# Performance work log

Hardware: AMD Instinct MI355X
Metric: run time of the kernel (lower is better)

## Reference

```python
import jax, jax.numpy as jnp
import numpy as np

N = 50000   # num entities
R2 = 480    # num_rels * 2
D = 200     # h_dim
T = 4       # sequence_len (graph snapshots)
E = 100000  # edges per snapshot
L = 2       # rgcn layers
SLOPE = (1.0 / 8.0 + 1.0 / 3.0) / 2.0  # deterministic rrelu (eval-mode expected slope)


def setup_inputs() -> dict:
    key = jax.random.key(0)
    ks = jax.random.split(key, 13)
    s = 1.0 / np.sqrt(D)
    w = lambda k, shp, sc: jax.random.normal(k, shp, dtype=jnp.float32) * sc
    return {
        "src": jax.random.randint(ks[0], (T, E), 0, N, dtype=jnp.int32),
        "dst": jax.random.randint(ks[1], (T, E), 0, N, dtype=jnp.int32),
        "etype": jax.random.randint(ks[2], (T, E), 0, R2, dtype=jnp.int32),
        "dynamic_emb": w(ks[3], (N, D), 1.0),
        "emb_rel": w(ks[4], (R2, D), s),
        "W_ih": w(ks[5], (3 * D, 2 * D), s),
        "W_hh": w(ks[6], (3 * D, D), s),
        "b_ih": jnp.zeros((3 * D,), jnp.float32),
        "b_hh": jnp.zeros((3 * D,), jnp.float32),
        "W_neighbor": w(ks[7], (L, D, D), s),
        "W_loop": w(ks[8], (L, D, D), s),
        "time_gate_weight": w(ks[9], (D, D), s),
        "time_gate_bias": jnp.zeros((D,), jnp.float32),
    }


def _l2norm(x):
    n = jnp.linalg.norm(x, axis=-1, keepdims=True)
    return x / jnp.maximum(n, 1e-12)


def _gru(x, hprev, W_ih, W_hh, b_ih, b_hh):
    gi = x @ W_ih.T + b_ih
    gh = hprev @ W_hh.T + b_hh
    ir, iz, inn = jnp.split(gi, 3, axis=-1)
    hr, hz, hn = jnp.split(gh, 3, axis=-1)
    r = jax.nn.sigmoid(ir + hr)
    z = jax.nn.sigmoid(iz + hz)
    n = jnp.tanh(inn + r * hn)
    return (1.0 - z) * n + z * hprev


def reference(src, dst, etype, dynamic_emb, emb_rel, W_ih, W_hh, b_ih, b_hh,
              W_neighbor, W_loop, time_gate_weight, time_gate_bias):
    h_init = _l2norm(dynamic_emb)  # layer_norm=True path (F.normalize)

    def step(carry, g):
        h, h0 = carry
        s, d_, et = g
        # per-relation mean of entity embeddings touching that relation (r_to_e spans)
        ent_idx = jnp.concatenate([s, d_])          # [2E]
        seg = jnp.concatenate([et, et])             # [2E]
        ssum = jax.ops.segment_sum(h[ent_idx], seg, num_segments=R2)
        cnt = jax.ops.segment_sum(jnp.ones_like(seg, jnp.float32), seg, num_segments=R2)
        x_mean = ssum / jnp.maximum(cnt, 1.0)[:, None]          # absent rels stay 0
        x_input = jnp.concatenate([emb_rel, x_mean], axis=1)    # [R2, 2D]
        h0 = _l2norm(_gru(x_input, h0, W_ih, W_hh, b_ih, b_hh))
        # UnionRGCNLayer x L: gather -> sum-aggregate -> norm + self-loop -> rrelu
        deg = jax.ops.segment_sum(jnp.ones_like(d_, jnp.float32), d_, num_segments=N)
        norm = 1.0 / jnp.maximum(deg, 1.0)
        hh = h
        for l in range(L):
            pre = hh[s] + h0[et]                                  # [E, D]
            agg = jax.ops.segment_sum(pre, d_, num_segments=N) @ W_neighbor[l]
            out = agg * norm[:, None] + hh @ W_loop[l]
            hh = jnp.where(out >= 0, out, out * SLOPE)            # rrelu (eval)
        cur = _l2norm(hh)
        tw = jax.nn.sigmoid(h @ time_gate_weight + time_gate_bias)
        h = tw * cur + (1.0 - tw) * h
        return (h, h0), h

    (_, _), hist = jax.lax.scan(step, (h_init, emb_rel), (src, dst, etype))
    return hist  # [T, N, D] history of evolved entity embeddings
```

## Files before the change

### kernel.cpp

```cpp
#include <hip/hip_runtime.h>
#include <math.h>

#define NE 50000
#define R2C 480
#define DD 200
#define TT 4
#define EE 100000
#define SLOPE 0.22916666666666666f

#define SCCH 8
#define EPB (256 * SCCH)
#define APAD 224
#define WPAD 224
#define WSZ (208 * WPAD)
#define DCH 4096
#define DNC ((NE + DCH - 1) / DCH)
#define RSPL 8

typedef short short8 __attribute__((ext_vector_type(8)));
typedef float float4v __attribute__((ext_vector_type(4)));

__device__ __forceinline__ float sigm(float x) { return 1.f / (1.f + expf(-x)); }

__device__ __forceinline__ short f2bf(float f) {
  union { float f; unsigned u; } v;
  v.f = f;
  unsigned r = v.u + 0x7fffu + ((v.u >> 16) & 1u);
  return (short)(r >> 16);
}


__global__ void init_h_kernel(const float* __restrict__ emb, float* __restrict__ h) {
  int n = blockIdx.x;
  int lane = threadIdx.x;
  size_t base = (size_t)n * DD;
  float v0 = emb[base + lane];
  float v1 = emb[base + 64 + lane];
  float v2 = emb[base + 128 + lane];
  float v3 = (lane < 8) ? emb[base + 192 + lane] : 0.f;
  float ss = v0 * v0 + v1 * v1 + v2 * v2 + v3 * v3;
#pragma unroll
  for (int off = 32; off; off >>= 1) ss += __shfl_down(ss, off);
  ss = __shfl(ss, 0);
  float inv = 1.f / fmaxf(sqrtf(ss), 1e-12f);
  h[base + lane] = v0 * inv;
  h[base + 64 + lane] = v1 * inv;
  h[base + 128 + lane] = v2 * inv;
  if (lane < 8) h[base + 192 + lane] = v3 * inv;
}

__global__ void copy_kernel(const float* __restrict__ a, float* __restrict__ b, int n) {
  int i = blockIdx.x * blockDim.x + threadIdx.x;
  if (i < n) b[i] = a[i];
}

__global__ void fill_x_kernel(const float* __restrict__ emb_rel, float* __restrict__ X) {
  int i = blockIdx.x * blockDim.x + threadIdx.x;
  if (i >= R2C * DD) return;
  int r = i / DD, d = i - r * DD;
  X[(size_t)r * 400 + d] = emb_rel[i];
}

__global__ void prep_w_kernel(const float* __restrict__ Wnb, const float* __restrict__ Wlp,
                              const float* __restrict__ Wtg, short* __restrict__ Wb) {
  int idx = blockIdx.x * 256 + threadIdx.x;
  if (idx >= 5 * WSZ) return;
  int m = idx / WSZ, rem = idx - m * WSZ;
  int n = rem / WPAD, k = rem - n * WPAD;
  const float* s;
  if (m == 0) s = Wnb;
  else if (m == 1) s = Wnb + DD * DD;
  else if (m == 2) s = Wlp;
  else if (m == 3) s = Wlp + DD * DD;
  else s = Wtg;
  float v = (n < DD && k < DD) ? s[(size_t)k * DD + n] : 0.f;
  Wb[idx] = f2bf(v);
}

__global__ __launch_bounds__(256) void hist_kernel(const int* __restrict__ et,
                                                   const int* __restrict__ dst,
                                                   int* __restrict__ et_hist,
                                                   int* __restrict__ deg_hist) {
  __shared__ int lh[R2C];
  int t = blockIdx.y;
  int tid = threadIdx.x;
  int e0 = blockIdx.x * EPB;
  for (int i = tid; i < R2C; i += 256) lh[i] = 0;
  __syncthreads();
#pragma unroll
  for (int c = 0; c < SCCH; c++) {
    int e = e0 + c * 256 + tid;
    if (e < EE) {
      atomicAdd(&lh[et[(size_t)t * EE + e]], 1);
      atomicAdd(&deg_hist[(size_t)t * NE + dst[(size_t)t * EE + e]], 1);
    }
  }
  __syncthreads();
  for (int i = tid; i < R2C; i += 256)
    if (lh[i]) atomicAdd(&et_hist[t * R2C + i], lh[i]);
}

__global__ void scan_rel_kernel(const int* __restrict__ et_hist, int* __restrict__ rowptr) {
  int t = blockIdx.x;
  int tid = threadIdx.x;
  __shared__ int s[512];
  int v = (tid < R2C) ? 2 * et_hist[t * R2C + tid] : 0;
  s[tid] = v;
  __syncthreads();
  for (int off = 1; off < 512; off <<= 1) {
    int x = (tid >= off) ? s[tid - off] : 0;
    __syncthreads();
    s[tid] += x;
    __syncthreads();
  }
  if (tid < R2C) rowptr[t * (R2C + 1) + tid] = s[tid] - v;
  if (tid == 0) rowptr[t * (R2C + 1) + R2C] = 2 * EE;
}

__global__ __launch_bounds__(256) void deg_partial_kernel(const int* __restrict__ deg_hist,
                                                          int* __restrict__ csum) {
  int t = blockIdx.y, c = blockIdx.x, tid = threadIdx.x;
  const int* dh = deg_hist + (size_t)t * NE;
  int base = c * DCH + tid * 16;
  int s = 0;
  if (base < NE) {
    int end = base + 16 > NE ? NE : base + 16;
    for (int i = base; i < end; i++) s += dh[i];
  }
  __shared__ int red[256];
  red[tid] = s;
  __syncthreads();
  for (int off = 128; off; off >>= 1) {
    if (tid < off) red[tid] += red[tid + off];
    __syncthreads();
  }
  if (tid == 0) csum[t * DNC + c] = red[0];
}

__global__ __launch_bounds__(256) void deg_emit_kernel(const int* __restrict__ deg_hist,
                                                       const int* __restrict__ csum,
                                                       int* __restrict__ rowptr,
                                                       float* __restrict__ normv) {
  int t = blockIdx.y, c = blockIdx.x, tid = threadIdx.x;
  const int* dh = deg_hist + (size_t)t * NE;
  __shared__ int scan[256];
  __shared__ int soff;
  int base = c * DCH + tid * 16;
  int s = 0;
  if (base < NE) {
    int end = base + 16 > NE ? NE : base + 16;
    for (int i = base; i < end; i++) s += dh[i];
  }
  scan[tid] = s;
  __syncthreads();
  for (int off = 1; off < 256; off <<= 1) {
    int x = (tid >= off) ? scan[tid - off] : 0;
    __syncthreads();
    scan[tid] += x;
    __syncthreads();
  }
  if (tid == 0) {
    int o = 0;
    for (int j = 0; j < c; j++) o += csum[t * DNC + j];
    soff = o;
  }
  __syncthreads();
  int run = soff + scan[tid] - s;
  if (base < NE) {
    int end = base + 16 > NE ? NE : base + 16;
    for (int i = base; i < end; i++) {
      int v = dh[i];
      rowptr[t * (NE + 1) + i] = run;
      normv[(size_t)t * NE + i] = 1.f / fmaxf((float)v, 1.f);
      run += v;
    }
  }
  if (c == 0 && tid == 0) rowptr[t * (NE + 1) + NE] = EE;
}

__global__ __launch_bounds__(256) void scatter_rel_kernel(const int* __restrict__ src,
                                                          const int* __restrict__ dst,
                                                          const int* __restrict__ et,
                                                          const int* __restrict__ rowptr,
                                                          int* __restrict__ cursor,
                                                          int* __restrict__ sorted_ent) {
  __shared__ int lcnt[R2C];
  __shared__ int lbase[R2C];
  int t = blockIdx.y;
  int tid = threadIdx.x;
  int e0 = blockIdx.x * EPB;
  for (int i = tid; i < R2C; i += 256) lcnt[i] = 0;
  __syncthreads();
  int rels[SCCH];
#pragma unroll
  for (int c = 0; c < SCCH; c++) {
    int e = e0 + c * 256 + tid;
    int r = (e < EE) ? et[(size_t)t * EE + e] : -1;
    rels[c] = r;
    if (r >= 0) atomicAdd(&lcnt[r], 2);
  }
  __syncthreads();
  const int* rp = rowptr + t * (R2C + 1);
  for (int i = tid; i < R2C; i += 256) {
    int c = lcnt[i];
    lbase[i] = rp[i] + (c ? atomicAdd(&cursor[t * R2C + i], c) : 0);
    lcnt[i] = 0;
  }
  __syncthreads();
  int* se = sorted_ent + (size_t)t * 2 * EE;
#pragma unroll
  for (int c = 0; c < SCCH; c++) {
    int r = rels[c];
    if (r >= 0) {
      int e = e0 + c * 256 + tid;
      int off = atomicAdd(&lcnt[r], 2);
      int p = lbase[r] + off;
      se[p] = src[(size_t)t * EE + e];
      se[p + 1] = dst[(size_t)t * EE + e];
    }
  }
}

__global__ void scatter_dst_kernel(const int* __restrict__ src, const int* __restrict__ dst,
                                   const int* __restrict__ et, const int* __restrict__ rowptr,
                                   int* __restrict__ cursor, int2* __restrict__ sorted_se) {
  int i = blockIdx.x * blockDim.x + threadIdx.x;
  if (i >= TT * EE) return;
  int t = i / EE;
  int d = dst[i];
  int base = rowptr[t * (NE + 1) + d];
  int p = base + atomicAdd(&cursor[(size_t)t * NE + d], 1);
  sorted_se[(size_t)t * EE + p] = make_int2(src[i], et[i]);
}


__global__ void relmean_part_kernel(const float* __restrict__ h, const int* __restrict__ rowptr,
                                    const int* __restrict__ sorted_ent_t,
                                    float* __restrict__ Xpart) {
  int r = blockIdx.x, j = blockIdx.y;
  int beg = rowptr[r], end = rowptr[r + 1];
  int lane = threadIdx.x & 63, w = threadIdx.x >> 6;
  float a0 = 0, a1 = 0, a2 = 0, a3 = 0;
  for (int i = beg + j * 4 + w; i < end; i += 4 * RSPL) {
    int idx = sorted_ent_t[i];
    const float* row = h + (size_t)idx * DD;
    a0 += row[lane];
    a1 += row[64 + lane];
    a2 += row[128 + lane];
    if (lane < 8) a3 += row[192 + lane];
  }
  __shared__ float part[4][DD];
  part[w][lane] = a0;
  part[w][64 + lane] = a1;
  part[w][128 + lane] = a2;
  if (lane < 8) part[w][192 + lane] = a3;
  __syncthreads();
  for (int d = threadIdx.x; d < DD; d += 256) {
    Xpart[((size_t)r * RSPL + j) * DD + d] = part[0][d] + part[1][d] + part[2][d] + part[3][d];
  }
}

__global__ void relmean_comb_kernel(const float* __restrict__ Xpart,
                                    const int* __restrict__ rowptr, float* __restrict__ X) {
  int r = blockIdx.x;
  int d = threadIdx.x;
  if (d >= DD) return;
  float s = 0.f;
#pragma unroll
  for (int j = 0; j < RSPL; j++) s += Xpart[((size_t)r * RSPL + j) * DD + d];
  float cnt = fmaxf((float)(rowptr[r + 1] - rowptr[r]), 1.f);
  X[(size_t)r * 400 + 200 + d] = s / cnt;
}

__global__ __launch_bounds__(256) void gemm_gru(const float* __restrict__ X,
                                                const float* __restrict__ h0,
                                                const float* __restrict__ W_ih,
                                                const float* __restrict__ W_hh,
                                                float* __restrict__ gi) {
  int z = blockIdx.z;
  const float* A = z ? h0 : X;
  const float* B = z ? W_hh : W_ih;
  float* C = gi + (size_t)z * R2C * 600;
  int K = z ? DD : 2 * DD;
  const int M = R2C, N = 600;
  __shared__ float As[32][33];
  __shared__ float Bs[32][33];
  int tid = threadIdx.x;
  int col0 = blockIdx.x * 32;
  int row0 = blockIdx.y * 32;
  int tr = tid >> 4, tc = tid & 15;
  float a00 = 0, a01 = 0, a10 = 0, a11 = 0;
  for (int k0 = 0; k0 < K; k0 += 32) {
    __syncthreads();
    for (int i = tid; i < 1024; i += 256) {
      int kk = i & 31, r = i >> 5;
      int row = row0 + r, k = k0 + kk;
      As[kk][r] = (row < M && k < K) ? A[(size_t)row * K + k] : 0.f;
    }
    for (int i = tid; i < 1024; i += 256) {
      int kk = i & 31, c = i >> 5;
      int col = col0 + c, k = k0 + kk;
      Bs[kk][c] = (col < N && k < K) ? B[(size_t)col * K + k] : 0.f;
    }
    __syncthreads();
#pragma unroll
    for (int kk = 0; kk < 32; kk++) {
      float x0 = As[kk][tr * 2], x1 = As[kk][tr * 2 + 1];
      float y0 = Bs[kk][tc * 2], y1 = Bs[kk][tc * 2 + 1];
      a00 += x0 * y0;
      a01 += x0 * y1;
      a10 += x1 * y0;
      a11 += x1 * y1;
    }
  }
  int row = row0 + tr * 2, col = col0 + tc * 2;
  if (row < M && col < N) C[(size_t)row * N + col] = a00;
  if (row < M && col + 1 < N) C[(size_t)row * N + col + 1] = a01;
  if (row + 1 < M && col < N) C[(size_t)(row + 1) * N + col] = a10;
  if (row + 1 < M && col + 1 < N) C[(size_t)(row + 1) * N + col + 1] = a11;
}

__global__ void gru_gate_kernel(const float* __restrict__ gi, const float* __restrict__ gh,
                                const float* __restrict__ b_ih, const float* __restrict__ b_hh,
                                float* __restrict__ h0) {
  int r = blockIdx.x;
  int tid = threadIdx.x;
  int lane = tid & 63, w = tid >> 6;
  __shared__ float red[4];
  float o = 0.f;
  if (tid < DD) {
    size_t b = (size_t)r * (3 * DD);
    float ir = gi[b + tid] + b_ih[tid];
    float iz = gi[b + DD + tid] + b_ih[DD + tid];
    float inn = gi[b + 2 * DD + tid] + b_ih[2 * DD + tid];
    float hr = gh[b + tid] + b_hh[tid];
    float hz = gh[b + DD + tid] + b_hh[DD + tid];
    float hn = gh[b + 2 * DD + tid] + b_hh[2 * DD + tid];
    float hv = h0[(size_t)r * DD + tid];
    float rr = sigm(ir + hr);
    float z = sigm(iz + hz);
    float n = tanhf(inn + rr * hn);
    o = (1.f - z) * n + z * hv;
  }
  float ss = o * o;
#pragma unroll
  for (int off = 32; off; off >>= 1) ss += __shfl_down(ss, off);
  if (lane == 0) red[w] = ss;
  __syncthreads();
  float tot = red[0] + red[1] + red[2] + red[3];
  float inv = 1.f / fmaxf(sqrtf(tot), 1e-12f);
  if (tid < DD) h0[(size_t)r * DD + tid] = o * inv;
}

__global__ void agg_kernel(const float* __restrict__ hh, const float* __restrict__ h0,
                           const int* __restrict__ rowptr, const int2* __restrict__ se_t,
                           const float* __restrict__ normv_t, short* __restrict__ aggb) {
  int w = threadIdx.x >> 6, lane = threadIdx.x & 63;
  int n = blockIdx.x * 4 + w;
  if (n >= NE) return;
  int beg = rowptr[n], end = rowptr[n + 1];
  float a0 = 0, a1 = 0, a2 = 0, a3 = 0;
  for (int i = beg; i < end; i++) {
    int2 p = se_t[i];
    const float* hr = hh + (size_t)p.x * DD;
    const float* qr = h0 + (size_t)p.y * DD;
    a0 += hr[lane] + qr[lane];
    a1 += hr[64 + lane] + qr[64 + lane];
    a2 += hr[128 + lane] + qr[128 + lane];
    if (lane < 8) a3 += hr[192 + lane] + qr[192 + lane];
  }
  float nm = normv_t[n];
  short* outp = aggb + (size_t)n * APAD;
  outp[lane] = f2bf(a0 * nm);
  outp[64 + lane] = f2bf(a1 * nm);
  outp[128 + lane] = f2bf(a2 * nm);
  if (lane < 8) outp[192 + lane] = f2bf(a3 * nm);
  else if (lane < 32) outp[192 + lane] = 0;
}


__global__ __launch_bounds__(256) void gemm_l0(const short* __restrict__ A1,
                                               const float* __restrict__ A2,
                                               const short* __restrict__ WbN,
                                               const short* __restrict__ WbL,
                                               const short* __restrict__ WbT,
                                               float* __restrict__ C, float* __restrict__ tg) {
  __shared__ short Bt[3][208][40];
  int tid = threadIdx.x;
  int lane = tid & 63, w = tid >> 6;
  int quad = lane >> 4, l16 = lane & 15;
  int row = blockIdx.x * 64 + w * 16 + l16;
  bool rok = row < NE;

  short8 af1[7], af2[7];
#pragma unroll
  for (int c = 0; c < 7; c++) {
    af1[c] = rok ? *(const short8*)(A1 + (size_t)row * APAD + c * 32 + quad * 8)
                 : (short8){0, 0, 0, 0, 0, 0, 0, 0};
  }
#pragma unroll
  for (int c = 0; c < 7; c++) {
    int kb = c * 32 + quad * 8;
    short8 a = (short8){0, 0, 0, 0, 0, 0, 0, 0};
    if (rok && kb < DD) {
      const float* ap = A2 + (size_t)row * DD + kb;
      float4v v0 = *(const float4v*)ap;
      float4v v1 = *(const float4v*)(ap + 4);
      short tmp[8] = {f2bf(v0[0]), f2bf(v0[1]), f2bf(v0[2]), f2bf(v0[3]),
                      f2bf(v1[0]), f2bf(v1[1]), f2bf(v1[2]), f2bf(v1[3])};
      a = *(short8*)&tmp[0];
    }
    af2[c] = a;
  }

  float4v accA[13], accT[13];
#pragma unroll
  for (int ct = 0; ct < 13; ct++) {
    accA[ct] = (float4v){0.f, 0.f, 0.f, 0.f};
    accT[ct] = (float4v){0.f, 0.f, 0.f, 0.f};
  }

#pragma unroll
  for (int c = 0; c < 7; c++) {
    __syncthreads();
#pragma unroll
    for (int it = 0; it < 10; it++) {
      int s = tid + it * 256;
      if (s < 2496) {
        int m = s / 832;
        int ss = s - m * 832;
        int n = ss % 208, k8 = (ss / 208) * 8;
        const short* Wb = (m == 0) ? WbN : (m == 1) ? WbL : WbT;
        *(short8*)&Bt[m][n][k8] = *(const short8*)&Wb[(size_t)n * WPAD + c * 32 + k8];
      }
    }
    __syncthreads();
#pragma unroll
    for (int ct = 0; ct < 13; ct++) {
      short8 b0 = *(short8*)&Bt[0][ct * 16 + l16][quad * 8];
      short8 b1 = *(short8*)&Bt[1][ct * 16 + l16][quad * 8];
      short8 b2 = *(short8*)&Bt[2][ct * 16 + l16][quad * 8];
      accA[ct] = __builtin_amdgcn_mfma_f32_16x16x32_bf16(af1[c], b0, accA[ct], 0, 0, 0);
      accA[ct] = __builtin_amdgcn_mfma_f32_16x16x32_bf16(af2[c], b1, accA[ct], 0, 0, 0);
      accT[ct] = __builtin_amdgcn_mfma_f32_16x16x32_bf16(af2[c], b2, accT[ct], 0, 0, 0);
    }
  }
  int r0 = blockIdx.x * 64 + w * 16 + quad * 4;
#pragma unroll
  for (int ct = 0; ct < 13; ct++) {
    int col = ct * 16 + l16;
    if (col >= DD) continue;
#pragma unroll
    for (int i = 0; i < 4; i++) {
      int r = r0 + i;
      if (r < NE) {
        float v = accA[ct][i];
        v = (v >= 0.f) ? v : v * SLOPE;
        C[(size_t)r * DD + col] = v;
        tg[(size_t)r * DD + col] = accT[ct][i];
      }
    }
  }
}

__global__ __launch_bounds__(256) void gemm_l1(const short* __restrict__ A1,
                                               const float* __restrict__ A2,
                                               const short* __restrict__ WbN,
                                               const short* __restrict__ WbL,
                                               const float* __restrict__ tg,
                                               const float* __restrict__ tgb,
                                               const float* __restrict__ hcur,
                                               float* __restrict__ outp) {
  __shared__ short Bt[2][208][40];
  int tid = threadIdx.x;
  int lane = tid & 63, w = tid >> 6;
  int quad = lane >> 4, l16 = lane & 15;
  int row = blockIdx.x * 64 + w * 16 + l16;
  bool rok = row < NE;

  short8 af1[7], af2[7];
#pragma unroll
  for (int c = 0; c < 7; c++) {
    af1[c] = rok ? *(const short8*)(A1 + (size_t)row * APAD + c * 32 + quad * 8)
                 : (short8){0, 0, 0, 0, 0, 0, 0, 0};
  }
#pragma unroll
  for (int c = 0; c < 7; c++) {
    int kb = c * 32 + quad * 8;
    short8 a = (short8){0, 0, 0, 0, 0, 0, 0, 0};
    if (rok && kb < DD) {
      const float* ap = A2 + (size_t)row * DD + kb;
      float4v v0 = *(const float4v*)ap;
      float4v v1 = *(const float4v*)(ap + 4);
      short tmp[8] = {f2bf(v0[0]), f2bf(v0[1]), f2bf(v0[2]), f2bf(v0[3]),
                      f2bf(v1[0]), f2bf(v1[1]), f2bf(v1[2]), f2bf(v1[3])};
      a = *(short8*)&tmp[0];
    }
    af2[c] = a;
  }

  float4v acc[13];
#pragma unroll
  for (int ct = 0; ct < 13; ct++) acc[ct] = (float4v){0.f, 0.f, 0.f, 0.f};

#pragma unroll
  for (int c = 0; c < 7; c++) {
    __syncthreads();
#pragma unroll
    for (int it = 0; it < 7; it++) {
      int s = tid + it * 256;
      if (s < 1664) {
        int m = s >= 832;
        int ss = s - m * 832;
        int n = ss % 208, k8 = (ss / 208) * 8;
        const short* Wb = m ? WbL : WbN;
        *(short8*)&Bt[m][n][k8] = *(const short8*)&Wb[(size_t)n * WPAD + c * 32 + k8];
      }
    }
    __syncthreads();
#pragma unroll
    for (int ct = 0; ct < 13; ct++) {
      short8 b1 = *(short8*)&Bt[0][ct * 16 + l16][quad * 8];
      short8 b2 = *(short8*)&Bt[1][ct * 16 + l16][quad * 8];
      acc[ct] = __builtin_amdgcn_mfma_f32_16x16x32_bf16(af1[c], b1, acc[ct], 0, 0, 0);
      acc[ct] = __builtin_amdgcn_mfma_f32_16x16x32_bf16(af2[c], b2, acc[ct], 0, 0, 0);
    }
  }
#pragma unroll
  for (int ct = 0; ct < 13; ct++)
#pragma unroll
    for (int i = 0; i < 4; i++) {
      float v = acc[ct][i];
      acc[ct][i] = (v >= 0.f) ? v : v * SLOPE;
    }
  int rbase = blockIdx.x * 64 + w * 16 + quad * 4;
#pragma unroll
  for (int i = 0; i < 4; i++) {
    int r = rbase + i;
    bool ok = r < NE;
    size_t rb = (size_t)r * DD;
    float ssq = 0.f;
#pragma unroll
    for (int ct = 0; ct < 13; ct++) {
      float x = acc[ct][i];
      ssq += x * x;
    }
#pragma unroll
    for (int off = 1; off < 16; off <<= 1) ssq += __shfl_xor(ssq, off);
    float inv = 1.f / fmaxf(sqrtf(ssq), 1e-12f);
#pragma unroll
    for (int ct = 0; ct < 13; ct++) {
      int col = ct * 16 + l16;
      if (ok && col < DD) {
        float cur = acc[ct][i] * inv;
        float tw = sigm(tg[rb + col] + tgb[col]);
        outp[rb + col] = tw * cur + (1.f - tw) * hcur[rb + col];
      }
    }
  }
}


extern "C" void kernel_launch(void* const* d_in, const int* in_sizes, int n_in, void* d_out,
                              int out_size, void* d_ws, size_t ws_size, hipStream_t stream) {
  const int* src = (const int*)d_in[0];
  const int* dst = (const int*)d_in[1];
  const int* et = (const int*)d_in[2];
  const float* dyn = (const float*)d_in[3];
  const float* emb_rel = (const float*)d_in[4];
  const float* W_ih = (const float*)d_in[5];
  const float* W_hh = (const float*)d_in[6];
  const float* b_ih = (const float*)d_in[7];
  const float* b_hh = (const float*)d_in[8];
  const float* W_nb = (const float*)d_in[9];
  const float* W_lp = (const float*)d_in[10];
  const float* Wtg = (const float*)d_in[11];
  const float* tgb = (const float*)d_in[12];
  float* out = (float*)d_out;

  char* p = (char*)d_ws;
  float* h = (float*)p;        p += (size_t)NE * DD * 4;
  float* bufB = (float*)p;     p += (size_t)NE * DD * 4;
  float* agg = (float*)p;      p += (size_t)NE * DD * 4;
  float* h0 = (float*)p;       p += (size_t)R2C * DD * 4;
  float* X = (float*)p;        p += (size_t)R2C * 400 * 4;
  float* normv = (float*)p;    p += (size_t)TT * NE * 4;
  int* et_rowptr = (int*)p;    p += (size_t)TT * (R2C + 1) * 4;
  int* et_cursor = (int*)p;    p += (size_t)TT * R2C * 4;
  int* et_hist = (int*)p;      p += (size_t)TT * R2C * 4;
  int* sorted_ent = (int*)p;   p += (size_t)TT * 2 * EE * 4;
  int* dst_rowptr = (int*)p;   p += (size_t)TT * (NE + 1) * 4;
  int* dst_cursor = (int*)p;   p += (size_t)TT * NE * 4;
  int* deg_hist = (int*)p;     p += (size_t)TT * NE * 4;
  int2* sorted_se = (int2*)p;  p += (size_t)TT * EE * 8;
  short* Wb = (short*)p;       p += (size_t)5 * WSZ * 2;
  float* Xpart = (float*)p;    p += (size_t)R2C * RSPL * DD * 4;
  int* csum = (int*)p;         p += (size_t)TT * DNC * 4;

  float* gi = bufB;
  float* gh = bufB + (size_t)R2C * 3 * DD;
  short* aggb = (short*)agg;
  float* tg = bufB;

  hipMemsetAsync(et_hist, 0, (size_t)TT * R2C * 4, stream);
  hipMemsetAsync(deg_hist, 0, (size_t)TT * NE * 4, stream);
  hipMemsetAsync(et_cursor, 0, (size_t)TT * R2C * 4, stream);
  hipMemsetAsync(dst_cursor, 0, (size_t)TT * NE * 4, stream);

  init_h_kernel<<<NE, 64, 0, stream>>>(dyn, h);
  copy_kernel<<<(R2C * DD + 255) / 256, 256, 0, stream>>>(emb_rel, h0, R2C * DD);
  fill_x_kernel<<<(R2C * DD + 255) / 256, 256, 0, stream>>>(emb_rel, X);
  prep_w_kernel<<<(5 * WSZ + 255) / 256, 256, 0, stream>>>(W_nb, W_lp, Wtg, Wb);
  const dim3 bin_grid((EE + EPB - 1) / EPB, TT);
  hist_kernel<<<bin_grid, 256, 0, stream>>>(et, dst, et_hist, deg_hist);
  scan_rel_kernel<<<TT, 512, 0, stream>>>(et_hist, et_rowptr);
  const dim3 deg_grid(DNC, TT);
  deg_partial_kernel<<<deg_grid, 256, 0, stream>>>(deg_hist, csum);
  deg_emit_kernel<<<deg_grid, 256, 0, stream>>>(deg_hist, csum, dst_rowptr, normv);
  scatter_rel_kernel<<<bin_grid, 256, 0, stream>>>(src, dst, et, et_rowptr, et_cursor, sorted_ent);
  scatter_dst_kernel<<<(TT * EE + 255) / 256, 256, 0, stream>>>(src, dst, et, dst_rowptr,
                                                                dst_cursor, sorted_se);

  const int gemm_grid = (NE + 63) / 64;
  const dim3 gru_grid((600 + 31) / 32, (R2C + 31) / 32, 2);
  const dim3 rm_grid(R2C, RSPL);
  for (int t = 0; t < TT; t++) {
    const float* hcur = (t == 0) ? h : out + (size_t)(t - 1) * NE * DD;
    float* bufA = out + (size_t)t * NE * DD;

    relmean_part_kernel<<<rm_grid, 256, 0, stream>>>(hcur, et_rowptr + t * (R2C + 1),
                                                     sorted_ent + (size_t)t * 2 * EE, Xpart);
    relmean_comb_kernel<<<R2C, 256, 0, stream>>>(Xpart, et_rowptr + t * (R2C + 1), X);
    gemm_gru<<<gru_grid, 256, 0, stream>>>(X, h0, W_ih, W_hh, gi);
    gru_gate_kernel<<<R2C, 256, 0, stream>>>(gi, gh, b_ih, b_hh, h0);
    agg_kernel<<<(NE + 3) / 4, 256, 0, stream>>>(hcur, h0, dst_rowptr + t * (NE + 1),
                                                 sorted_se + (size_t)t * EE,
                                                 normv + (size_t)t * NE, aggb);
    gemm_l0<<<gemm_grid, 256, 0, stream>>>(aggb, hcur, Wb + 0 * WSZ, Wb + 2 * WSZ, Wb + 4 * WSZ,
                                           bufA, tg);
    agg_kernel<<<(NE + 3) / 4, 256, 0, stream>>>(bufA, h0, dst_rowptr + t * (NE + 1),
                                                 sorted_se + (size_t)t * EE,
                                                 normv + (size_t)t * NE, aggb);
    gemm_l1<<<gemm_grid, 256, 0, stream>>>(aggb, bufA, Wb + 1 * WSZ, Wb + 3 * WSZ, tg, tgb, hcur,
                                           bufA);
  }
}
```

Measured before the change: 1.494 ms.

## Pre-swizzle weights into MFMA fragment layout and drop LDS staging in GEMMs

Weights are now prepacked once into a per-lane MFMA B-fragment order, so each GEMM lane loads its fragment straight from global memory. This removes the shared-memory tile staging and both __syncthreads per K chunk. The time-gate GEMM moves out of the layer-0 kernel into its own gemm_tg kernel. That shrinks accumulator register pressure in the layer-0 kernel but adds one launch and a second read of hcur per step.

```diff
diff --git a/kernel.cpp b/kernel.cpp
--- a/kernel.cpp
+++ b/kernel.cpp
@@ -11,8 +11,7 @@
 #define SCCH 8
 #define EPB (256 * SCCH)
 #define APAD 224
-#define WPAD 224
-#define WSZ (208 * WPAD)
+#define WSZ (7 * 13 * 512)
 #define DCH 4096
 #define DNC ((NE + DCH - 1) / DCH)
 #define RSPL 8
@@ -62,19 +61,25 @@
 }
 
 __global__ void prep_w_kernel(const float* __restrict__ Wnb, const float* __restrict__ Wlp,
-                              const float* __restrict__ Wtg, short* __restrict__ Wb) {
+                              const float* __restrict__ Wtg, short* __restrict__ Wf) {
   int idx = blockIdx.x * 256 + threadIdx.x;
   if (idx >= 5 * WSZ) return;
   int m = idx / WSZ, rem = idx - m * WSZ;
-  int n = rem / WPAD, k = rem - n * WPAD;
+  int blk = rem >> 9;
+  int within = rem & 511;
+  int lane = within >> 3, j = within & 7;
+  int c = blk / 13, ct = blk - c * 13;
+  int l16 = lane & 15, quad = lane >> 4;
+  int col = ct * 16 + l16;
+  int k = c * 32 + quad * 8 + j;
   const float* s;
   if (m == 0) s = Wnb;
   else if (m == 1) s = Wnb + DD * DD;
   else if (m == 2) s = Wlp;
   else if (m == 3) s = Wlp + DD * DD;
   else s = Wtg;
-  float v = (n < DD && k < DD) ? s[(size_t)k * DD + n] : 0.f;
-  Wb[idx] = f2bf(v);
+  float v = (col < DD && k < DD) ? s[(size_t)k * DD + col] : 0.f;
+  Wf[idx] = f2bf(v);
 }
 
 __global__ __launch_bounds__(256) void hist_kernel(const int* __restrict__ et,
@@ -379,13 +384,19 @@
 }
 
 
-__global__ __launch_bounds__(256) void gemm_l0(const short* __restrict__ A1,
-                                               const float* __restrict__ A2,
-                                               const short* __restrict__ WbN,
-                                               const short* __restrict__ WbL,
-                                               const short* __restrict__ WbT,
-                                               float* __restrict__ C, float* __restrict__ tg) {
-  __shared__ short Bt[3][208][40];
+__device__ __forceinline__ short8 ldA_f32(const float* __restrict__ ap) {
+  float4v v0 = *(const float4v*)ap;
+  float4v v1 = *(const float4v*)(ap + 4);
+  short tmp[8] = {f2bf(v0[0]), f2bf(v0[1]), f2bf(v0[2]), f2bf(v0[3]),
+                  f2bf(v1[0]), f2bf(v1[1]), f2bf(v1[2]), f2bf(v1[3])};
+  return *(short8*)&tmp[0];
+}
+
+__global__ __launch_bounds__(256) void gemm_dual(const short* __restrict__ A1,
+                                                 const short* __restrict__ Wf1,
+                                                 const float* __restrict__ A2,
+                                                 const short* __restrict__ Wf2,
+                                                 float* __restrict__ C) {
   int tid = threadIdx.x;
   int lane = tid & 63, w = tid >> 6;
   int quad = lane >> 4, l16 = lane & 15;
@@ -394,55 +405,30 @@
 
   short8 af1[7], af2[7];
 #pragma unroll
-  for (int c = 0; c < 7; c++) {
+  for (int c = 0; c < 7; c++)
     af1[c] = rok ? *(const short8*)(A1 + (size_t)row * APAD + c * 32 + quad * 8)
                  : (short8){0, 0, 0, 0, 0, 0, 0, 0};
-  }
 #pragma unroll
   for (int c = 0; c < 7; c++) {
     int kb = c * 32 + quad * 8;
-    short8 a = (short8){0, 0, 0, 0, 0, 0, 0, 0};
-    if (rok && kb < DD) {
-      const float* ap = A2 + (size_t)row * DD + kb;
-      float4v v0 = *(const float4v*)ap;
-      float4v v1 = *(const float4v*)(ap + 4);
-      short tmp[8] = {f2bf(v0[0]), f2bf(v0[1]), f2bf(v0[2]), f2bf(v0[3]),
-                      f2bf(v1[0]), f2bf(v1[1]), f2bf(v1[2]), f2bf(v1[3])};
-      a = *(short8*)&tmp[0];
-    }
-    af2[c] = a;
-  }
-
-  float4v accA[13], accT[13];
-#pragma unroll
-  for (int ct = 0; ct < 13; ct++) {
-    accA[ct] = (float4v){0.f, 0.f, 0.f, 0.f};
-    accT[ct] = (float4v){0.f, 0.f, 0.f, 0.f};
-  }
-
+    af2[c] = (rok && kb < DD) ? ldA_f32(A2 + (size_t)row * DD + kb)
+                              : (short8){0, 0, 0, 0, 0, 0, 0, 0};
+  }
+
+  float4v acc[13];
+#pragma unroll
+  for (int ct = 0; ct < 13; ct++) acc[ct] = (float4v){0.f, 0.f, 0.f, 0.f};
+
+  const short* wf1 = Wf1 + lane * 8;
+  const short* wf2 = Wf2 + lane * 8;
 #pragma unroll
   for (int c = 0; c < 7; c++) {
-    __syncthreads();
-#pragma unroll
-    for (int it = 0; it < 10; it++) {
-      int s = tid + it * 256;
-      if (s < 2496) {
-        int m = s / 832;
-        int ss = s - m * 832;
-        int n = ss % 208, k8 = (ss / 208) * 8;
-        const short* Wb = (m == 0) ? WbN : (m == 1) ? WbL : WbT;
-        *(short8*)&Bt[m][n][k8] = *(const short8*)&Wb[(size_t)n * WPAD + c * 32 + k8];
-      }
-    }
-    __syncthreads();
 #pragma unroll
     for (int ct = 0; ct < 13; ct++) {
-      short8 b0 = *(short8*)&Bt[0][ct * 16 + l16][quad * 8];
-      short8 b1 = *(short8*)&Bt[1][ct * 16 + l16][quad * 8];
-      short8 b2 = *(short8*)&Bt[2][ct * 16 + l16][quad * 8];
-      accA[ct] = __builtin_amdgcn_mfma_f32_16x16x32_bf16(af1[c], b0, accA[ct], 0, 0, 0);
-      accA[ct] = __builtin_amdgcn_mfma_f32_16x16x32_bf16(af2[c], b1, accA[ct], 0, 0, 0);
-      accT[ct] = __builtin_amdgcn_mfma_f32_16x16x32_bf16(af2[c], b2, accT[ct], 0, 0, 0);
+      short8 b1 = *(const short8*)(wf1 + (size_t)(c * 13 + ct) * 512);
+      short8 b2 = *(const short8*)(wf2 + (size_t)(c * 13 + ct) * 512);
+      acc[ct] = __builtin_amdgcn_mfma_f32_16x16x32_bf16(af1[c], b1, acc[ct], 0, 0, 0);
+      acc[ct] = __builtin_amdgcn_mfma_f32_16x16x32_bf16(af2[c], b2, acc[ct], 0, 0, 0);
     }
   }
   int r0 = blockIdx.x * 64 + w * 16 + quad * 4;
@@ -454,74 +440,95 @@
     for (int i = 0; i < 4; i++) {
       int r = r0 + i;
       if (r < NE) {
-        float v = accA[ct][i];
+        float v = acc[ct][i];
         v = (v >= 0.f) ? v : v * SLOPE;
         C[(size_t)r * DD + col] = v;
-        tg[(size_t)r * DD + col] = accT[ct][i];
       }
     }
   }
 }
 
-__global__ __launch_bounds__(256) void gemm_l1(const short* __restrict__ A1,
-                                               const float* __restrict__ A2,
-                                               const short* __restrict__ WbN,
-                                               const short* __restrict__ WbL,
-                                               const float* __restrict__ tg,
-                                               const float* __restrict__ tgb,
-                                               const float* __restrict__ hcur,
-                                               float* __restrict__ outp) {
-  __shared__ short Bt[2][208][40];
+__global__ __launch_bounds__(256) void gemm_tg(const float* __restrict__ A,
+                                               const short* __restrict__ WfT,
+                                               float* __restrict__ tg) {
   int tid = threadIdx.x;
   int lane = tid & 63, w = tid >> 6;
   int quad = lane >> 4, l16 = lane & 15;
   int row = blockIdx.x * 64 + w * 16 + l16;
   bool rok = row < NE;
 
+  short8 af[7];
+#pragma unroll
+  for (int c = 0; c < 7; c++) {
+    int kb = c * 32 + quad * 8;
+    af[c] = (rok && kb < DD) ? ldA_f32(A + (size_t)row * DD + kb)
+                             : (short8){0, 0, 0, 0, 0, 0, 0, 0};
+  }
+
+  float4v acc[13];
+#pragma unroll
+  for (int ct = 0; ct < 13; ct++) acc[ct] = (float4v){0.f, 0.f, 0.f, 0.f};
+
+  const short* wf = WfT + lane * 8;
+#pragma unroll
+  for (int c = 0; c < 7; c++) {
+#pragma unroll
+    for (int ct = 0; ct < 13; ct++) {
+      short8 b = *(const short8*)(wf + (size_t)(c * 13 + ct) * 512);
+      acc[ct] = __builtin_amdgcn_mfma_f32_16x16x32_bf16(af[c], b, acc[ct], 0, 0, 0);
+    }
+  }
+  int r0 = blockIdx.x * 64 + w * 16 + quad * 4;
+#pragma unroll
+  for (int ct = 0; ct < 13; ct++) {
+    int col = ct * 16 + l16;
+    if (col >= DD) continue;
+#pragma unroll
+    for (int i = 0; i < 4; i++) {
+      int r = r0 + i;
+      if (r < NE) tg[(size_t)r * DD + col] = acc[ct][i];
+    }
+  }
+}
+
+__global__ __launch_bounds__(256) void gemm_l1fin(const short* __restrict__ A1,
+                                                  const float* __restrict__ A2,
+                                                  const short* __restrict__ WfN,
+                                                  const short* __restrict__ WfL,
+                                                  const float* __restrict__ tg,
+                                                  const float* __restrict__ tgb,
+                                                  const float* __restrict__ hcur,
+                                                  float* __restrict__ outp) {
+  int tid = threadIdx.x;
+  int lane = tid & 63, w = tid >> 6;
+  int quad = lane >> 4, l16 = lane & 15;
+  int row = blockIdx.x * 64 + w * 16 + l16;
+  bool rok = row < NE;
+
   short8 af1[7], af2[7];
 #pragma unroll
-  for (int c = 0; c < 7; c++) {
+  for (int c = 0; c < 7; c++)
     af1[c] = rok ? *(const short8*)(A1 + (size_t)row * APAD + c * 32 + quad * 8)
                  : (short8){0, 0, 0, 0, 0, 0, 0, 0};
-  }
 #pragma unroll
   for (int c = 0; c < 7; c++) {
     int kb = c * 32 + quad * 8;
-    short8 a = (short8){0, 0, 0, 0, 0, 0, 0, 0};
-    if (rok && kb < DD) {
-      const float* ap = A2 + (size_t)row * DD + kb;
-      float4v v0 = *(const float4v*)ap;
-      float4v v1 = *(const float4v*)(ap + 4);
-      short tmp[8] = {f2bf(v0[0]), f2bf(v0[1]), f2bf(v0[2]), f2bf(v0[3]),
-                      f2bf(v1[0]), f2bf(v1[1]), f2bf(v1[2]), f2bf(v1[3])};
-      a = *(short8*)&tmp[0];
-    }
-    af2[c] = a;
+    af2[c] = (rok && kb < DD) ? ldA_f32(A2 + (size_t)row * DD + kb)
+                              : (short8){0, 0, 0, 0, 0, 0, 0, 0};
   }
 
   float4v acc[13];
 #pragma unroll
   for (int ct = 0; ct < 13; ct++) acc[ct] = (float4v){0.f, 0.f, 0.f, 0.f};
 
+  const short* wfn = WfN + lane * 8;
+  const short* wfl = WfL + lane * 8;
 #pragma unroll
   for (int c = 0; c < 7; c++) {
-    __syncthreads();
-#pragma unroll
-    for (int it = 0; it < 7; it++) {
-      int s = tid + it * 256;
-      if (s < 1664) {
-        int m = s >= 832;
-        int ss = s - m * 832;
-        int n = ss % 208, k8 = (ss / 208) * 8;
-        const short* Wb = m ? WbL : WbN;
-        *(short8*)&Bt[m][n][k8] = *(const short8*)&Wb[(size_t)n * WPAD + c * 32 + k8];
-      }
-    }
-    __syncthreads();
 #pragma unroll
     for (int ct = 0; ct < 13; ct++) {
-      short8 b1 = *(short8*)&Bt[0][ct * 16 + l16][quad * 8];
-      short8 b2 = *(short8*)&Bt[1][ct * 16 + l16][quad * 8];
+      short8 b1 = *(const short8*)(wfn + (size_t)(c * 13 + ct) * 512);
+      short8 b2 = *(const short8*)(wfl + (size_t)(c * 13 + ct) * 512);
       acc[ct] = __builtin_amdgcn_mfma_f32_16x16x32_bf16(af1[c], b1, acc[ct], 0, 0, 0);
       acc[ct] = __builtin_amdgcn_mfma_f32_16x16x32_bf16(af2[c], b2, acc[ct], 0, 0, 0);
     }
@@ -593,7 +600,7 @@
   int* dst_cursor = (int*)p;   p += (size_t)TT * NE * 4;
   int* deg_hist = (int*)p;     p += (size_t)TT * NE * 4;
   int2* sorted_se = (int2*)p;  p += (size_t)TT * EE * 8;
-  short* Wb = (short*)p;       p += (size_t)5 * WSZ * 2;
+  short* Wf = (short*)p;       p += (size_t)5 * WSZ * 2;
   float* Xpart = (float*)p;    p += (size_t)R2C * RSPL * DD * 4;
   int* csum = (int*)p;         p += (size_t)TT * DNC * 4;
 
@@ -610,7 +617,7 @@
   init_h_kernel<<<NE, 64, 0, stream>>>(dyn, h);
   copy_kernel<<<(R2C * DD + 255) / 256, 256, 0, stream>>>(emb_rel, h0, R2C * DD);
   fill_x_kernel<<<(R2C * DD + 255) / 256, 256, 0, stream>>>(emb_rel, X);
-  prep_w_kernel<<<(5 * WSZ + 255) / 256, 256, 0, stream>>>(W_nb, W_lp, Wtg, Wb);
+  prep_w_kernel<<<(5 * WSZ + 255) / 256, 256, 0, stream>>>(W_nb, W_lp, Wtg, Wf);
   const dim3 bin_grid((EE + EPB - 1) / EPB, TT);
   hist_kernel<<<bin_grid, 256, 0, stream>>>(et, dst, et_hist, deg_hist);
   scan_rel_kernel<<<TT, 512, 0, stream>>>(et_hist, et_rowptr);
@@ -633,15 +640,15 @@
     relmean_comb_kernel<<<R2C, 256, 0, stream>>>(Xpart, et_rowptr + t * (R2C + 1), X);
     gemm_gru<<<gru_grid, 256, 0, stream>>>(X, h0, W_ih, W_hh, gi);
     gru_gate_kernel<<<R2C, 256, 0, stream>>>(gi, gh, b_ih, b_hh, h0);
+    gemm_tg<<<gemm_grid, 256, 0, stream>>>(hcur, Wf + 4 * WSZ, tg);
     agg_kernel<<<(NE + 3) / 4, 256, 0, stream>>>(hcur, h0, dst_rowptr + t * (NE + 1),
                                                  sorted_se + (size_t)t * EE,
                                                  normv + (size_t)t * NE, aggb);
-    gemm_l0<<<gemm_grid, 256, 0, stream>>>(aggb, hcur, Wb + 0 * WSZ, Wb + 2 * WSZ, Wb + 4 * WSZ,
-                                           bufA, tg);
+    gemm_dual<<<gemm_grid, 256, 0, stream>>>(aggb, Wf + 0 * WSZ, hcur, Wf + 2 * WSZ, bufA);
     agg_kernel<<<(NE + 3) / 4, 256, 0, stream>>>(bufA, h0, dst_rowptr + t * (NE + 1),
                                                  sorted_se + (size_t)t * EE,
                                                  normv + (size_t)t * NE, aggb);
-    gemm_l1<<<gemm_grid, 256, 0, stream>>>(aggb, bufA, Wb + 1 * WSZ, Wb + 3 * WSZ, tg, tgb, hcur,
-                                           bufA);
-  }
-}
+    gemm_l1fin<<<gemm_grid, 256, 0, stream>>>(aggb, bufA, Wf + 1 * WSZ, Wf + 3 * WSZ, tg, tgb,
+                                              hcur, bufA);
+  }
+}
```

Result: faster. 1.458 ms (-2.4%).
